# Performance work log

Hardware: AMD Instinct MI355X
Metric: run time of the kernel (lower is better)

## Reference

```python
import jax, jax.numpy as jnp
import numpy as np

B, S, H = 2, 2048, 256
NS, NR = 512, 512
FFN_RATIO = 4


def setup_inputs() -> dict:
    key = jax.random.key(0)
    ks = jax.random.split(key, 8)
    token_reps = jax.random.normal(ks[0], (B, S, H), dtype=jnp.float32)
    token_masks = jnp.ones((B, S), dtype=bool)
    span_reps = jax.random.normal(ks[1], (B, NS, H), dtype=jnp.float32)
    # spans: start in [0, S-16), length in [1, 16) -> valid [start, end) windows
    starts = jax.random.randint(ks[2], (B, NS), 0, S - 16)
    lens = jax.random.randint(ks[3], (B, NS), 1, 16)
    span_ids = jnp.stack([starts, starts + lens], axis=-1)  # (B, NS, 2)
    rel_ids = jax.random.randint(ks[4], (B, NR, 2), 0, NS)  # (B, NR, 2)
    rel_masks = jnp.ones((B, NR), dtype=bool)
    neg_limit = jnp.float32(-6.0e4)
    d_in = 3 * H
    d_ff = FFN_RATIO * d_in
    W1 = jax.random.normal(ks[5], (d_in, d_ff), dtype=jnp.float32) / np.float32(np.sqrt(d_in))
    b1 = jnp.zeros((d_ff,), dtype=jnp.float32)
    W2 = jax.random.normal(ks[6], (d_ff, H), dtype=jnp.float32) / np.float32(np.sqrt(d_ff))
    b2 = jnp.zeros((H,), dtype=jnp.float32)
    return {
        "token_reps": token_reps, "token_masks": token_masks,
        "span_reps": span_reps, "span_ids": span_ids,
        "rel_ids": rel_ids, "rel_masks": rel_masks, "neg_limit": neg_limit,
        "W1": W1, "b1": b1, "W2": W2, "b2": b2,
    }


def reference(token_reps, token_masks, span_reps, span_ids, rel_ids, rel_masks,
              neg_limit, W1, b1, W2, b2):
    seq_len = token_reps.shape[1]
    head_ids = rel_ids[..., 0]  # (B, NR)
    tail_ids = rel_ids[..., 1]
    # gather head/tail span reps: (B, NR, H)
    head_reps = jnp.take_along_axis(span_reps, head_ids[..., None], axis=1)
    tail_reps = jnp.take_along_axis(span_reps, tail_ids[..., None], axis=1)
    # span boundaries per relation: (B, NR)
    head_start = jnp.take_along_axis(span_ids[..., 0], head_ids, axis=1)
    head_end = jnp.take_along_axis(span_ids[..., 1], head_ids, axis=1)
    tail_start = jnp.take_along_axis(span_ids[..., 0], tail_ids, axis=1)
    tail_end = jnp.take_along_axis(span_ids[..., 1], tail_ids, axis=1)
    seq = jnp.arange(seq_len)[None, None, :]  # (1, 1, S)
    head_m = (seq >= head_start[..., None]) & (seq < head_end[..., None])
    tail_m = (seq >= tail_start[..., None]) & (seq < tail_end[..., None])
    # 'between' base context: tokens strictly between the two spans
    lo = jnp.minimum(head_end, tail_end)[..., None]
    hi = jnp.maximum(head_start, tail_start)[..., None]
    base = (seq >= lo) & (seq < hi)
    ctx_mask = base & ~(head_m | tail_m) & rel_masks[..., None] & token_masks[:, None, :]  # (B, NR, S)
    # masked max-pool over seq: (B, NR, S, H) -> (B, NR, H)
    masked = jnp.where(ctx_mask[..., None], token_reps[:, None, :, :], neg_limit)
    context_reps = jnp.max(masked, axis=2)
    # no-context fallback: fully-masked relations -> zero vector
    all_masked = jnp.all(context_reps == neg_limit, axis=-1)
    context_reps = jnp.where(all_masked[..., None], jnp.float32(0.0), context_reps)
    rel_reps = jnp.concatenate([head_reps, tail_reps, context_reps], axis=-1)  # (B, NR, 3H)
    h = jax.nn.relu(rel_reps @ W1 + b1)  # dropout = identity at inference
    return h @ W2 + b2
```

## Files before the change

kernel.cpp:

```cpp
#include <hip/hip_runtime.h>
#include <hip/hip_bf16.h>
#include <stdint.h>

#define Bb 2
#define Ss 2048
#define Hh 256
#define NSs 512
#define NRr 512
#define DIN 768
#define DFF 3072
#define Mm (Bb*NRr)

typedef __attribute__((ext_vector_type(8))) short short8;
typedef __attribute__((ext_vector_type(4))) short short4b;
typedef __attribute__((ext_vector_type(4))) float floatx4;
typedef __attribute__((ext_vector_type(2))) float floatx2;

__device__ __forceinline__ short f2bf(float f) {
  uint32_t u = __float_as_uint(f);
  u += 0x7fffu + ((u >> 16) & 1u);
  return (short)(u >> 16);
}

__device__ __forceinline__ short4b f2bf4(floatx4 v) {
  short4b r;
  r.x = f2bf(v.x); r.y = f2bf(v.y); r.z = f2bf(v.z); r.w = f2bf(v.w);
  return r;
}

__device__ __forceinline__ uint32_t pack_bf2_rne(float lo, float hi) {
  uint32_t ul = __float_as_uint(lo); ul += 0x7fffu + ((ul >> 16) & 1u);
  uint32_t uh = __float_as_uint(hi); uh += 0x7fffu + ((uh >> 16) & 1u);
  return (uh & 0xffff0000u) | (ul >> 16);
}

__device__ __forceinline__ uint32_t max_packed(uint32_t a, uint32_t b) {
  float a0 = __uint_as_float(a << 16), a1 = __uint_as_float(a & 0xffff0000u);
  float b0 = __uint_as_float(b << 16), b1 = __uint_as_float(b & 0xffff0000u);
  float m0 = fmaxf(a0, b0), m1 = fmaxf(a1, b1);
  return (__float_as_uint(m1) & 0xffff0000u) | (__float_as_uint(m0) >> 16);
}

__device__ __forceinline__ void gld_lds16(const void* g, void* l) {
  __builtin_amdgcn_global_load_lds(
      (const __attribute__((address_space(1))) void*)g,
      (__attribute__((address_space(3))) void*)l, 16, 0, 0);
}

__global__ __launch_bounds__(256) void prep_all(
    const float* __restrict__ token_reps,
    const float* __restrict__ span_reps,
    const int* __restrict__ span_ids,
    const int* __restrict__ rel_ids,
    short* __restrict__ X,
    const float* __restrict__ W1, short* __restrict__ W1t,
    const float* __restrict__ W2, short* __restrict__ W2t)
{
  __shared__ __align__(16) uint32_t LvRaw[8 * Ss];
  int bid = blockIdx.x;
  int t = threadIdx.x;

  if (bid < 256) {
    uint32_t (*Lv)[Ss] = (uint32_t(*)[Ss])LvRaw;
    int b = bid >> 7;
    int r7 = bid & 127;
    int L = ((r7 >> 6) & 1) * 8 + (r7 & 7);
    int m = (r7 >> 3) & 7;
    int g = L * 8 + m;
    int c2 = g * 2;

#pragma unroll
    for (int j = 0; j < 8; ++j) {
      int i = j * 256 + t;
      floatx2 v = *(const floatx2*)&token_reps[((size_t)b * Ss + i) * Hh + c2];
      Lv[0][i] = pack_bf2_rne(v.x, v.y);
    }
    __syncthreads();
#pragma unroll
    for (int k = 1; k <= 7; ++k) {
      int d = 1 << (k - 1);
#pragma unroll
      for (int j = 0; j < 8; ++j) {
        int i = j * 256 + t;
        Lv[k][i] = max_packed(Lv[k - 1][i], Lv[k - 1][min(i + d, Ss - 1)]);
      }
      __syncthreads();
    }

#pragma unroll
    for (int rr = 0; rr < 2; ++rr) {
      int r = rr * 256 + t;
      int hid = rel_ids[(b * NRr + r) * 2 + 0];
      int tid_ = rel_ids[(b * NRr + r) * 2 + 1];
      int hs = span_ids[(b * NSs + hid) * 2 + 0];
      int he = span_ids[(b * NSs + hid) * 2 + 1];
      int ts = span_ids[(b * NSs + tid_) * 2 + 0];
      int te = span_ids[(b * NSs + tid_) * 2 + 1];
      int lo = min(he, te), hi = max(hs, ts);
      int s1 = hs, e1 = he, s2 = ts, e2 = te;
      if (s2 < s1) { s1 = ts; e1 = te; s2 = hs; e2 = he; }

      int ia[3], ibv[3], ni = 0;
      if (e1 >= s2) {
        int me = max(e1, e2);
        int a = lo, bb2 = min(hi, s1); if (a < bb2) { ia[ni]=a; ibv[ni]=bb2; ni++; }
        a = max(lo, me); bb2 = hi;     if (a < bb2) { ia[ni]=a; ibv[ni]=bb2; ni++; }
      } else {
        int a = lo, bb2 = min(hi, s1);      if (a < bb2) { ia[ni]=a; ibv[ni]=bb2; ni++; }
        a = max(lo, e1); bb2 = min(hi, s2); if (a < bb2) { ia[ni]=a; ibv[ni]=bb2; ni++; }
        a = max(lo, e2); bb2 = hi;          if (a < bb2) { ia[ni]=a; ibv[ni]=bb2; ni++; }
      }

      uint32_t acc = 0xff80ff80u;
      for (int q = 0; q < ni; ++q) {
        int a = ia[q], e = ibv[q], len = e - a;
        if (len >= 128) {
          int x = a;
          for (; x + 128 <= e; x += 128) acc = max_packed(acc, Lv[7][x]);
          if (x < e) acc = max_packed(acc, Lv[7][e - 128]);
        } else {
          int k = 31 - __builtin_clz(len);
          acc = max_packed(acc, Lv[k][a]);
          acc = max_packed(acc, Lv[k][e - (1 << k)]);
        }
      }
      if (ni == 0) acc = 0;
      *(uint32_t*)&X[(size_t)(b * NRr + r) * DIN + 2 * Hh + c2] = acc;
    }
  } else if (bid < 512) {
    int w = t >> 6, lane = t & 63;
    int br = (bid - 256) * 4 + w;
    int b = br >> 9, r = br & (NRr - 1);
    int hid = rel_ids[(b * NRr + r) * 2 + 0];
    int tid_ = rel_ids[(b * NRr + r) * 2 + 1];
    int c4 = lane * 4;
    floatx4 hr = *(const floatx4*)&span_reps[((size_t)b * NSs + hid) * Hh + c4];
    floatx4 tr = *(const floatx4*)&span_reps[((size_t)b * NSs + tid_) * Hh + c4];
    size_t base = (size_t)br * DIN;
    *(short4b*)&X[base + c4]      = f2bf4(hr);
    *(short4b*)&X[base + Hh + c4] = f2bf4(tr);
  } else {
    float (*tile)[33] = (float(*)[33])LvRaw;
    int cb = bid - 512;
    const float* W; short* Wt; int K, N, bx, by;
    if (cb < 2304) { W = W1; Wt = W1t; K = DIN; N = DFF; bx = cb % 96; by = cb / 96; }
    else { cb -= 2304; W = W2; Wt = W2t; K = DFF; N = Hh; bx = cb % 8; by = cb / 8; }
    int n0 = bx * 32, k0 = by * 32;
    int tx = t & 31, ty = t >> 5;
#pragma unroll
    for (int i = 0; i < 4; ++i)
      tile[ty + i * 8][tx] = W[(size_t)(k0 + ty + i * 8) * N + n0 + tx];
    __syncthreads();
#pragma unroll
    for (int i = 0; i < 4; ++i)
      Wt[(size_t)(n0 + ty + i * 8) * K + k0 + tx] = f2bf(tile[tx][ty + i * 8]);
  }
}

template <int BM, int BN, bool RELU_BF16>
__global__ __launch_bounds__(256) void gemm_bt(
    const short* __restrict__ A, const short* __restrict__ Bt,
    const float* __restrict__ bias, void* __restrict__ Cout,
    int M, int N, int K) {
  constexpr int BK = 32;
  constexpr int WM = BM / 2, WN = BN / 2;
  constexpr int MT = WM / 16, NT = WN / 16;
  __shared__ __align__(16) short As[BM * BK];
  __shared__ __align__(16) short Bs[BN * BK];

  int tid = threadIdx.x;
  int lane = tid & 63, w = tid >> 6;
  int wi = w & 1, wj = w >> 1;
  int m0 = blockIdx.x * BM, n0 = blockIdx.y * BN;
  int quad = lane >> 4, l16 = lane & 15;

  floatx4 acc[MT][NT];
#pragma unroll
  for (int i = 0; i < MT; ++i)
#pragma unroll
    for (int j = 0; j < NT; ++j)
      acc[i][j] = (floatx4){0.f, 0.f, 0.f, 0.f};

  constexpr int ACH = BM / 16;
  constexpr int BCH = BN / 16;

  for (int kk = 0; kk < K; kk += BK) {
#pragma unroll
    for (int i = 0; i < ACH / 4; ++i) {
      int chunk = w * (ACH / 4) + i;
      int r = chunk * 16 + (lane >> 2);
      gld_lds16(A + (size_t)(m0 + r) * K + kk + (lane & 3) * 8, &As[chunk * 512]);
    }
#pragma unroll
    for (int i = 0; i < BCH / 4; ++i) {
      int chunk = w * (BCH / 4) + i;
      int r = chunk * 16 + (lane >> 2);
      gld_lds16(Bt + (size_t)(n0 + r) * K + kk + (lane & 3) * 8, &Bs[chunk * 512]);
    }
    __syncthreads();

    short8 a[MT], b[NT];
#pragma unroll
    for (int i = 0; i < MT; ++i)
      a[i] = *(const short8*)&As[(wi * WM + i * 16 + l16) * BK + quad * 8];
#pragma unroll
    for (int j = 0; j < NT; ++j)
      b[j] = *(const short8*)&Bs[(wj * WN + j * 16 + l16) * BK + quad * 8];
#pragma unroll
    for (int i = 0; i < MT; ++i)
#pragma unroll
      for (int j = 0; j < NT; ++j)
        acc[i][j] = __builtin_amdgcn_mfma_f32_16x16x32_bf16(a[i], b[j],
                                                            acc[i][j], 0, 0, 0);
    __syncthreads();
  }

#pragma unroll
  for (int i = 0; i < MT; ++i) {
#pragma unroll
    for (int j = 0; j < NT; ++j) {
      int col = n0 + wj * WN + j * 16 + l16;
      float bv = bias[col];
#pragma unroll
      for (int rr = 0; rr < 4; ++rr) {
        int row = m0 + wi * WM + i * 16 + quad * 4 + rr;
        float v = acc[i][j][rr] + bv;
        if (RELU_BF16) {
          v = fmaxf(v, 0.f);
          ((short*)Cout)[(size_t)row * N + col] = f2bf(v);
        } else {
          ((float*)Cout)[(size_t)row * N + col] = v;
        }
      }
    }
  }
}

__global__ __launch_bounds__(256) void gemm2_wsk(
    const short* __restrict__ A,
    const short* __restrict__ Bt,
    const float* __restrict__ bias,
    float* __restrict__ out)
{
  constexpr int K = DFF, N = Hh;
  __shared__ __align__(16) short S[4][2][2][1024];
  int tid = threadIdx.x, lane = tid & 63, w = tid >> 6;
  int m0 = (blockIdx.x >> 3) * 32, n0 = (blockIdx.x & 7) * 32;
  int quad = lane >> 4, l16 = lane & 15;
  int kb = w * (K / 4);
  int r = lane >> 2;
  int co = (lane & 3) * 8;

  floatx4 acc[2][2];
#pragma unroll
  for (int i = 0; i < 2; ++i)
#pragma unroll
    for (int j = 0; j < 2; ++j)
      acc[i][j] = (floatx4){0.f, 0.f, 0.f, 0.f};

  {
    short* As = &S[w][0][0][0];
    short* Bs = &S[w][0][1][0];
    gld_lds16(A + (size_t)(m0 + r) * K + kb + co, As);
    gld_lds16(A + (size_t)(m0 + 16 + r) * K + kb + co, As + 512);
    gld_lds16(Bt + (size_t)(n0 + r) * K + kb + co, Bs);
    gld_lds16(Bt + (size_t)(n0 + 16 + r) * K + kb + co, Bs + 512);
  }

  for (int it = 0; it < 24; ++it) {
    int buf = it & 1;
    if (it + 1 < 24) {
      int kk = kb + (it + 1) * 32;
      short* As = &S[w][buf ^ 1][0][0];
      short* Bs = &S[w][buf ^ 1][1][0];
      gld_lds16(A + (size_t)(m0 + r) * K + kk + co, As);
      gld_lds16(A + (size_t)(m0 + 16 + r) * K + kk + co, As + 512);
      gld_lds16(Bt + (size_t)(n0 + r) * K + kk + co, Bs);
      gld_lds16(Bt + (size_t)(n0 + 16 + r) * K + kk + co, Bs + 512);
      asm volatile("s_waitcnt vmcnt(4)" ::: "memory");
    } else {
      asm volatile("s_waitcnt vmcnt(0)" ::: "memory");
    }
    const short* As = &S[w][buf][0][0];
    const short* Bs = &S[w][buf][1][0];
    short8 a[2], b[2];
#pragma unroll
    for (int i = 0; i < 2; ++i)
      a[i] = *(const short8*)&As[(i * 16 + l16) * 32 + quad * 8];
#pragma unroll
    for (int j = 0; j < 2; ++j)
      b[j] = *(const short8*)&Bs[(j * 16 + l16) * 32 + quad * 8];
#pragma unroll
    for (int i = 0; i < 2; ++i)
#pragma unroll
      for (int j = 0; j < 2; ++j)
        acc[i][j] = __builtin_amdgcn_mfma_f32_16x16x32_bf16(a[i], b[j],
                                                            acc[i][j], 0, 0, 0);
  }

  float* red = (float*)&S[w][0][0][0];
#pragma unroll
  for (int i = 0; i < 2; ++i)
#pragma unroll
    for (int j = 0; j < 2; ++j)
#pragma unroll
      for (int rr = 0; rr < 4; ++rr)
        red[(i * 16 + quad * 4 + rr) * 32 + (j * 16 + l16)] = acc[i][j][rr];
  __syncthreads();

  int e = tid * 4;
  int row = e >> 5, col = e & 31;
  floatx4 s = *(const floatx4*)&bias[n0 + col];
#pragma unroll
  for (int w2 = 0; w2 < 4; ++w2)
    s += *(const floatx4*)&((const float*)&S[w2][0][0][0])[e];
  *(floatx4*)&out[(size_t)(m0 + row) * N + n0 + col] = s;
}

__global__ __launch_bounds__(256) void ctx_kernel(
    const float* __restrict__ token_reps,
    const float* __restrict__ span_reps,
    const int* __restrict__ span_ids,
    const int* __restrict__ rel_ids,
    short* __restrict__ X)
{
  int br = blockIdx.x;
  int b = br >> 9;
  int r = br & (NRr - 1);
  int c = threadIdx.x;
  int hid = rel_ids[(b * NRr + r) * 2 + 0];
  int tid = rel_ids[(b * NRr + r) * 2 + 1];
  int hs = span_ids[(b * NSs + hid) * 2 + 0];
  int he = span_ids[(b * NSs + hid) * 2 + 1];
  int ts = span_ids[(b * NSs + tid) * 2 + 0];
  int te = span_ids[(b * NSs + tid) * 2 + 1];
  int lo = min(he, te);
  int hi = max(hs, ts);
  float m = -3.4e38f;
  bool found = false;
  const float* tr = token_reps + ((size_t)b * Ss) * Hh + c;
  for (int s = lo; s < hi; ++s) {
    bool inspan = (s >= hs && s < he) || (s >= ts && s < te);
    if (!inspan) { found = true; m = fmaxf(m, tr[(size_t)s * Hh]); }
  }
  float ctx = found ? m : 0.0f;
  size_t base = (size_t)br * DIN;
  X[base + c]          = f2bf(span_reps[((size_t)b * NSs + hid) * Hh + c]);
  X[base + Hh + c]     = f2bf(span_reps[((size_t)b * NSs + tid) * Hh + c]);
  X[base + 2 * Hh + c] = f2bf(ctx);
}

__global__ void convT(const float* __restrict__ W, short* __restrict__ Wt,
                      int K, int N) {
  __shared__ float tile[32][33];
  int n0 = blockIdx.x * 32, k0 = blockIdx.y * 32;
  int tx = threadIdx.x, ty = threadIdx.y;
#pragma unroll
  for (int i = 0; i < 4; ++i)
    tile[ty + i * 8][tx] = W[(size_t)(k0 + ty + i * 8) * N + n0 + tx];
  __syncthreads();
#pragma unroll
  for (int i = 0; i < 4; ++i)
    Wt[(size_t)(n0 + ty + i * 8) * K + k0 + tx] = f2bf(tile[tx][ty + i * 8]);
}

extern "C" void kernel_launch(void* const* d_in, const int* in_sizes, int n_in,
                              void* d_out, int out_size, void* d_ws,
                              size_t ws_size, hipStream_t stream) {
  const float*   token_reps  = (const float*)d_in[0];
  const float*   span_reps   = (const float*)d_in[2];
  const int*     span_ids    = (const int*)d_in[3];
  const int*     rel_ids     = (const int*)d_in[4];
  const float*   W1 = (const float*)d_in[7];
  const float*   b1 = (const float*)d_in[8];
  const float*   W2 = (const float*)d_in[9];
  const float*   b2 = (const float*)d_in[10];
  float* out = (float*)d_out;

  char* ws = (char*)d_ws;
  short* X    = (short*)ws;
  short* W1t  = X + (size_t)Mm * DIN;
  short* W2t  = W1t + (size_t)DFF * DIN;
  short* hbuf = W2t + (size_t)Hh * DFF;
  size_t bf16_elems = (size_t)Mm * DIN + (size_t)DFF * DIN +
                      (size_t)Hh * DFF + (size_t)Mm * DFF;
  size_t need = bf16_elems * sizeof(short);

  bool fast = (ws_size >= need);
  if (fast) {
    hipLaunchKernelGGL(prep_all, dim3(512 + 2304 + 768), dim3(256), 0, stream,
                       token_reps, span_reps, span_ids, rel_ids, X,
                       W1, W1t, W2, W2t);
    hipLaunchKernelGGL((gemm_bt<64, 128, true>), dim3(Mm / 64, DFF / 128),
                       dim3(256), 0, stream, X, W1t, b1, (void*)hbuf,
                       Mm, DFF, DIN);
    hipLaunchKernelGGL(gemm2_wsk, dim3(256), dim3(256), 0, stream,
                       hbuf, W2t, b2, out);
  } else {
    hipLaunchKernelGGL(ctx_kernel, dim3(Mm), dim3(256), 0, stream,
                       token_reps, span_reps, span_ids, rel_ids, X);
    hipLaunchKernelGGL(convT, dim3(DFF / 32, DIN / 32), dim3(32, 8), 0, stream,
                       W1, W1t, DIN, DFF);
    hipLaunchKernelGGL(convT, dim3(Hh / 32, DFF / 32), dim3(32, 8), 0, stream,
                       W2, W2t, DFF, Hh);
    hipLaunchKernelGGL((gemm_bt<64, 128, true>), dim3(Mm / 64, DFF / 128),
                       dim3(256), 0, stream, X, W1t, b1, (void*)hbuf,
                       Mm, DFF, DIN);
    hipLaunchKernelGGL((gemm_bt<64, 64, false>), dim3(Mm / 64, Hh / 64),
                       dim3(256), 0, stream, hbuf, W2t, b2, (void*)out,
                       Mm, Hh, DFF);
  }
}
```

Measured before the change: 118.4 us.

## Retile GEMM1 to 64x96 and rewrite GEMM2 split-K to direct register loads

The first GEMM's tile moves from 64x128 to 64x96, which gives more blocks (16x32 instead of 16x24) to fill the GPU. Its load loop now spreads A and B chunks round-robin over the four waves so that non-multiple-of-4 chunk counts still work. The second GEMM drops the LDS double buffering and loads MFMA operands straight from global memory into registers. It uses 32x16 output tiles over 512 blocks, still split along K across the four waves and reduced through shared memory. This removes LDS staging and the waits that go with it, at the cost of uncoalesced per-lane global loads and no prefetch overlap.

```diff
diff --git a/kernel.cpp b/kernel.cpp
--- a/kernel.cpp
+++ b/kernel.cpp
@@ -183,19 +183,20 @@
 
   constexpr int ACH = BM / 16;
   constexpr int BCH = BN / 16;
+  constexpr int TCH = ACH + BCH;
+  int srow = lane >> 2, scol = (lane & 3) * 8;
 
   for (int kk = 0; kk < K; kk += BK) {
 #pragma unroll
-    for (int i = 0; i < ACH / 4; ++i) {
-      int chunk = w * (ACH / 4) + i;
-      int r = chunk * 16 + (lane >> 2);
-      gld_lds16(A + (size_t)(m0 + r) * K + kk + (lane & 3) * 8, &As[chunk * 512]);
-    }
-#pragma unroll
-    for (int i = 0; i < BCH / 4; ++i) {
-      int chunk = w * (BCH / 4) + i;
-      int r = chunk * 16 + (lane >> 2);
-      gld_lds16(Bt + (size_t)(n0 + r) * K + kk + (lane & 3) * 8, &Bs[chunk * 512]);
+    for (int c = 0; c < TCH; ++c) {
+      if ((c & 3) == w) {
+        if (c < ACH)
+          gld_lds16(A + (size_t)(m0 + c * 16 + srow) * K + kk + scol,
+                    &As[c * 512]);
+        else
+          gld_lds16(Bt + (size_t)(n0 + (c - ACH) * 16 + srow) * K + kk + scol,
+                    &Bs[(c - ACH) * 512]);
+      }
     }
     __syncthreads();
 
@@ -236,85 +237,48 @@
   }
 }
 
-__global__ __launch_bounds__(256) void gemm2_wsk(
+__global__ __launch_bounds__(256) void gemm2_reg(
     const short* __restrict__ A,
     const short* __restrict__ Bt,
     const float* __restrict__ bias,
     float* __restrict__ out)
 {
   constexpr int K = DFF, N = Hh;
-  __shared__ __align__(16) short S[4][2][2][1024];
+  __shared__ float red[4][32 * 16];
   int tid = threadIdx.x, lane = tid & 63, w = tid >> 6;
-  int m0 = (blockIdx.x >> 3) * 32, n0 = (blockIdx.x & 7) * 32;
+  int m0 = (blockIdx.x >> 4) * 32, n0 = (blockIdx.x & 15) * 16;
   int quad = lane >> 4, l16 = lane & 15;
   int kb = w * (K / 4);
-  int r = lane >> 2;
-  int co = (lane & 3) * 8;
-
-  floatx4 acc[2][2];
-#pragma unroll
-  for (int i = 0; i < 2; ++i)
-#pragma unroll
-    for (int j = 0; j < 2; ++j)
-      acc[i][j] = (floatx4){0.f, 0.f, 0.f, 0.f};
-
-  {
-    short* As = &S[w][0][0][0];
-    short* Bs = &S[w][0][1][0];
-    gld_lds16(A + (size_t)(m0 + r) * K + kb + co, As);
-    gld_lds16(A + (size_t)(m0 + 16 + r) * K + kb + co, As + 512);
-    gld_lds16(Bt + (size_t)(n0 + r) * K + kb + co, Bs);
-    gld_lds16(Bt + (size_t)(n0 + 16 + r) * K + kb + co, Bs + 512);
-  }
-
+
+  const short* a0p = A + (size_t)(m0 + l16) * K + kb + quad * 8;
+  const short* a1p = a0p + (size_t)16 * K;
+  const short* bp  = Bt + (size_t)(n0 + l16) * K + kb + quad * 8;
+
+  floatx4 acc0 = {0.f, 0.f, 0.f, 0.f};
+  floatx4 acc1 = {0.f, 0.f, 0.f, 0.f};
+#pragma unroll
   for (int it = 0; it < 24; ++it) {
-    int buf = it & 1;
-    if (it + 1 < 24) {
-      int kk = kb + (it + 1) * 32;
-      short* As = &S[w][buf ^ 1][0][0];
-      short* Bs = &S[w][buf ^ 1][1][0];
-      gld_lds16(A + (size_t)(m0 + r) * K + kk + co, As);
-      gld_lds16(A + (size_t)(m0 + 16 + r) * K + kk + co, As + 512);
-      gld_lds16(Bt + (size_t)(n0 + r) * K + kk + co, Bs);
-      gld_lds16(Bt + (size_t)(n0 + 16 + r) * K + kk + co, Bs + 512);
-      asm volatile("s_waitcnt vmcnt(4)" ::: "memory");
-    } else {
-      asm volatile("s_waitcnt vmcnt(0)" ::: "memory");
-    }
-    const short* As = &S[w][buf][0][0];
-    const short* Bs = &S[w][buf][1][0];
-    short8 a[2], b[2];
-#pragma unroll
-    for (int i = 0; i < 2; ++i)
-      a[i] = *(const short8*)&As[(i * 16 + l16) * 32 + quad * 8];
-#pragma unroll
-    for (int j = 0; j < 2; ++j)
-      b[j] = *(const short8*)&Bs[(j * 16 + l16) * 32 + quad * 8];
-#pragma unroll
-    for (int i = 0; i < 2; ++i)
-#pragma unroll
-      for (int j = 0; j < 2; ++j)
-        acc[i][j] = __builtin_amdgcn_mfma_f32_16x16x32_bf16(a[i], b[j],
-                                                            acc[i][j], 0, 0, 0);
-  }
-
-  float* red = (float*)&S[w][0][0][0];
-#pragma unroll
-  for (int i = 0; i < 2; ++i)
-#pragma unroll
-    for (int j = 0; j < 2; ++j)
-#pragma unroll
-      for (int rr = 0; rr < 4; ++rr)
-        red[(i * 16 + quad * 4 + rr) * 32 + (j * 16 + l16)] = acc[i][j][rr];
+    short8 a0 = *(const short8*)(a0p + it * 32);
+    short8 a1 = *(const short8*)(a1p + it * 32);
+    short8 b  = *(const short8*)(bp  + it * 32);
+    acc0 = __builtin_amdgcn_mfma_f32_16x16x32_bf16(a0, b, acc0, 0, 0, 0);
+    acc1 = __builtin_amdgcn_mfma_f32_16x16x32_bf16(a1, b, acc1, 0, 0, 0);
+  }
+
+#pragma unroll
+  for (int rr = 0; rr < 4; ++rr) {
+    red[w][(quad * 4 + rr) * 16 + l16]        = acc0[rr];
+    red[w][(16 + quad * 4 + rr) * 16 + l16]   = acc1[rr];
+  }
   __syncthreads();
 
-  int e = tid * 4;
-  int row = e >> 5, col = e & 31;
-  floatx4 s = *(const floatx4*)&bias[n0 + col];
+  int e = tid * 2;
+  int orow = e >> 4, ocol = e & 15;
+  floatx2 s = *(const floatx2*)&bias[n0 + ocol];
 #pragma unroll
   for (int w2 = 0; w2 < 4; ++w2)
-    s += *(const floatx4*)&((const float*)&S[w2][0][0][0])[e];
-  *(floatx4*)&out[(size_t)(m0 + row) * N + n0 + col] = s;
+    s += *(const floatx2*)&red[w2][e];
+  *(floatx2*)&out[(size_t)(m0 + orow) * N + n0 + ocol] = s;
 }
 
 __global__ __launch_bounds__(256) void ctx_kernel(
@@ -391,10 +355,10 @@
     hipLaunchKernelGGL(prep_all, dim3(512 + 2304 + 768), dim3(256), 0, stream,
                        token_reps, span_reps, span_ids, rel_ids, X,
                        W1, W1t, W2, W2t);
-    hipLaunchKernelGGL((gemm_bt<64, 128, true>), dim3(Mm / 64, DFF / 128),
+    hipLaunchKernelGGL((gemm_bt<64, 96, true>), dim3(Mm / 64, DFF / 96),
                        dim3(256), 0, stream, X, W1t, b1, (void*)hbuf,
                        Mm, DFF, DIN);
-    hipLaunchKernelGGL(gemm2_wsk, dim3(256), dim3(256), 0, stream,
+    hipLaunchKernelGGL(gemm2_reg, dim3(512), dim3(256), 0, stream,
                        hbuf, W2t, b2, out);
   } else {
     hipLaunchKernelGGL(ctx_kernel, dim3(Mm), dim3(256), 0, stream,
```

Result: slower. 127.0 us (+7.3%).
